# Kernel optimization log

Hardware: AMD Instinct MI355X
Metric: run time of the kernel (lower is better)

The kernel has to match this reference:

```python
import jax, jax.numpy as jnp
import numpy as np
from jax import lax

PATCH = 16
DILATIONS = (1, 2, 4, 8)
R2_THRESH = 0.5


def setup_inputs() -> dict:
    key = jax.random.key(0)
    k1, k2, k3 = jax.random.split(key, 3)
    seasonal = jax.random.normal(k1, (32, 2048, 8), dtype=jnp.float32)
    # 4 Conv1d(1,1,k=16) kernels + biases (PyTorch default init scale ~1/sqrt(k))
    conv_w = jax.random.normal(k2, (4, PATCH), dtype=jnp.float32) / np.sqrt(PATCH).astype(np.float32)
    conv_b = jax.random.normal(k3, (4,), dtype=jnp.float32) * 0.01
    return {"seasonal": seasonal, "conv_w": conv_w, "conv_b": conv_b}


def _r2(y):
    n = y.shape[-1]
    x = jnp.arange(n, dtype=y.dtype)
    xm = x - x.mean()                                  # [2p]
    ym = y - y.mean(axis=-1, keepdims=True)            # [..., 2p]
    sxy = jnp.einsum('...k,k->...', ym, xm)
    sxx = jnp.sum(xm * xm)
    syy = jnp.sum(ym * ym, axis=-1)
    return (sxy * sxy) / (sxx * syy)


def _forward(seasonal, conv_w, conv_b):
    B, S, C = seasonal.shape
    p = PATCH
    # channels are processed independently with the SAME convs -> fuse B and C
    x = seasonal.transpose(0, 2, 1).reshape(B * C, 1, S)  # [BC,1,S]
    win = jnp.arange(S - p + 1)[:, None] + jnp.arange(p)[None, :]  # [n_patches,p]
    cand_list = []
    for i, d in enumerate(DILATIONS):
        pad = (p - 1) * d
        out = lax.conv_general_dilated(
            x, conv_w[i].reshape(1, 1, p), window_strides=(1,),
            padding=[(pad, pad)], rhs_dilation=(d,)) + conv_b[i]
        out = out[:, 0, :S]                      # crop to seq_len, [BC,S]
        cand_list.append(out[:, win])            # sliding windows [BC,n_patches,p]
    cand = jnp.concatenate(cand_list, axis=1)    # [BC,N,p]
    N = cand.shape[1]

    # r^2 score for every adjacent pair (vectorized; greedy scan only gates it)
    pair = jnp.concatenate([cand[:, :-1], cand[:, 1:]], axis=-1)  # [BC,N-1,2p]
    can_merge = jnp.pad(_r2(pair) >= R2_THRESH, ((0, 0), (0, 1)),
                        constant_values=False)   # [BC,N]; last idx never merges

    # greedy sequential merge: if pair (i,i+1) merges, i+1 is consumed
    def step(consumed, cm_i):
        merge = jnp.logical_and(~consumed, cm_i)
        return merge, (merge, ~consumed)

    def scan_one(cm):
        _, (merge, valid) = lax.scan(step, jnp.zeros((), jnp.bool_), cm)
        return merge, valid

    merge, valid = jax.vmap(scan_one)(can_merge)  # [BC,N] each

    nxt = jnp.concatenate([cand[:, 1:], cand[:, -1:]], axis=1)
    outs = jnp.where(merge[..., None], 0.5 * (cand + nxt), cand)  # [BC,N,p]

    # pack selected patches to the front (stable order), zero-pad the tail
    order = jnp.argsort(~valid, axis=1)  # jax argsort is stable; valid first
    packed = jnp.take_along_axis(outs, order[..., None], axis=1)
    vmask = jnp.take_along_axis(valid, order, axis=1)
    packed = packed * vmask[..., None].astype(packed.dtype)

    return packed.reshape(B, C, N, p).transpose(0, 2, 3, 1)  # [B,N,p,C]


def reference(seasonal, conv_w, conv_b):
    return _forward(seasonal, conv_w, conv_b)
```

## Files before the change

### kernel.cpp

```cpp
#include <hip/hip_runtime.h>

#define SLEN 2048
#define PATCH 16
#define ND 4
#define NW 2033
#define NCAND 8132
#define NROWS 256
#define NCH 8
#define ROWPAD 8192


#define CDX(x) ((x) + ((x) >> 4))
#define XSX(x) ((x) + ((x) >> 3))

__global__ __launch_bounds__(512) void k1(
    const float* __restrict__ seasonal,
    const float* __restrict__ conv_w,
    const float* __restrict__ conv_b,
    float* __restrict__ convf,
    unsigned short* __restrict__ sel)
{
    const int row = blockIdx.x;
    const int b = row >> 3, c = row & 7;
    const int tid = threadIdx.x;

    __shared__ float  xs[XSX(SLEN-1)+1];
    __shared__ double cd[CDX(ND*SLEN-1)+1];
    __shared__ unsigned char c0s[512];
    __shared__ int      wmax[8];
    __shared__ unsigned wsum[8];

    for (int j = tid; j < SLEN; j += 512)
        xs[XSX(j)] = seasonal[(size_t)(b*SLEN + j)*NCH + c];
    __syncthreads();

    for (int d = 0; d < ND; ++d) {
        const int dil = 1 << d;
        double w[PATCH];
        #pragma unroll
        for (int k = 0; k < PATCH; ++k) w[k] = (double)conv_w[d*PATCH + k];
        const double bias = (double)conv_b[d];
        const int r  = tid & (dil - 1);
        const int g  = tid >> d;
        const int bx = g*4*dil + r;

        double xt[19];
        #pragma unroll
        for (int q = 0; q < 19; ++q) {
            int idx = bx + (q - 15)*dil;
            xt[q] = (idx >= 0) ? (double)xs[XSX(idx)] : 0.0;
        }
        double acc[4];
        #pragma unroll
        for (int m = 0; m < 4; ++m) acc[m] = 0.0;
        if (g >= 4) {
            #pragma unroll
            for (int m = 0; m < 4; ++m)
                #pragma unroll
                for (int k = 0; k < PATCH; ++k)
                    acc[m] += w[k] * xt[m + k];
        } else {
            #pragma unroll
            for (int m = 0; m < 4; ++m)
                #pragma unroll
                for (int k = 0; k < PATCH; ++k)
                    if (4*g + m + k - 15 >= 0)
                        acc[m] += w[k] * xt[m + k];
        }
        const int ob = d*SLEN + bx;
        #pragma unroll
        for (int m = 0; m < 4; ++m)
            cd[CDX(ob + m*dil)] = acc[m] + bias;
    }
    __syncthreads();

    {
        float* dst = convf + (size_t)row * ROWPAD;
        #pragma unroll
        for (int j = 0; j < 4; ++j) {
            int i4 = (tid + j*512) * 4;
            float4 v;
            v.x = (float)cd[CDX(i4+0)];
            v.y = (float)cd[CDX(i4+1)];
            v.z = (float)cd[CDX(i4+2)];
            v.w = (float)cd[CDX(i4+3)];
            *(float4*)&dst[i4] = v;
        }
    }

    unsigned char* cmL = (unsigned char*)xs;
    {
        const int d  = tid >> 7;
        const int u  = tid & 127;
        const int db = d * SLEN;
        if (u < 127) {
            const int w0 = u * 16;
            double W1=0.0, W2=0.0, Wk=0.0;
            #pragma unroll
            for (int k = 0; k < 16; ++k) {
                double v = cd[CDX(db + w0 + k)];
                W1 += v; W2 = fma(v,v,W2); Wk = fma((double)k,v,Wk);
            }
            unsigned char* crow = cmL + d*NW;
            #pragma unroll
            for (int j = 0; j < 16; ++j) {
                double v0 = cd[CDX(db+w0+j)], v16 = cd[CDX(db+w0+j+16)];
                double nW1 = W1 + (v16 - v0);
                double nW2 = W2 + (v16*v16 - v0*v0);
                double nWk = Wk - W1 + v0 + 15.0*v16;
                double S1  = W1 + nW1;
                double S2  = W2 + nW2;
                double Sxy = (Wk - 15.5*W1) + (nWk + 0.5*nW1);
                double syy = S2 - S1*S1*(1.0/32.0);
                crow[w0+j] = (unsigned char)((Sxy*Sxy >= 1364.0*syy) && (syy > 0.0));
                W1 = nW1; W2 = nW2; Wk = nWk;
            }
        } else if (d < 3) {
            double aW1=0,aW2=0,aWk=0, bW1=0,bW2=0,bWk=0;
            #pragma unroll
            for (int k = 0; k < 16; ++k) {
                double va = cd[CDX(db + 2032 + k)];
                double vb = cd[CDX(db + SLEN + k)];
                aW1 += va; aW2 = fma(va,va,aW2); aWk = fma((double)k,va,aWk);
                bW1 += vb; bW2 = fma(vb,vb,bW2); bWk = fma((double)k,vb,bWk);
            }
            double S1  = aW1 + bW1;
            double S2  = aW2 + bW2;
            double Sxy = (aWk - 15.5*aW1) + (bWk + 0.5*bW1);
            double syy = S2 - S1*S1*(1.0/32.0);
            cmL[d*NW + 2032] = (unsigned char)((Sxy*Sxy >= 1364.0*syy) && (syy > 0.0));
        }
        if (tid < 61) cmL[NCAND - 1 + tid] = 0;
    }
    __syncthreads();

    const int base = tid * 16;
    unsigned cmbits = 0;
    {
        const unsigned* cw = (const unsigned*)cmL;
        #pragma unroll
        for (int q = 0; q < 4; ++q) {
            unsigned wrd = cw[tid*4 + q];
            #pragma unroll
            for (int bb = 0; bb < 4; ++bb) {
                unsigned bit = ((wrd >> (8*bb)) & 0xffu) ? 1u : 0u;
                cmbits |= bit << (q*4 + bb);
            }
        }
    }
    unsigned inv16 = (~cmbits) & 0xffffu;
    const bool allones = (inv16 == 0u);
    unsigned T = allones ? 16u : (unsigned)__clz(inv16 << 16);
    c0s[tid] = (unsigned char)(T & 1u);
    int pm = allones ? -1 : tid;

    const int lane = tid & 63, wid = tid >> 6;
    int mscan = pm;
    #pragma unroll
    for (int off = 1; off < 64; off <<= 1) {
        int v = __shfl_up(mscan, off);
        if (lane >= off && v > mscan) mscan = v;
    }
    if (lane == 63) wmax[wid] = mscan;
    __syncthreads();
    int pshift = __shfl_up(mscan, 1);
    int mexcl = (lane == 0) ? -1 : pshift;
    #pragma unroll
    for (int wq = 0; wq < 8; ++wq)
        if (wq < wid) { int v = wmax[wq]; if (v > mexcl) mexcl = v; }
    unsigned carry = (mexcl >= 0) ? (unsigned)c0s[mexcl] : 0u;

    int nelem = NCAND - base; if (nelem > 16) nelem = 16; if (nelem < 0) nelem = 0;
    unsigned cons = carry, validb = 0, mergeb = 0;
    int cnt = 0;
    for (int w2 = 0; w2 < nelem; ++w2) {
        unsigned bit = (cmbits >> w2) & 1u;
        unsigned val = cons ^ 1u;
        unsigned mrg = bit & val;
        validb |= val << w2;
        mergeb |= mrg << w2;
        cnt += (int)val;
        cons = mrg;
    }

    int sscan = cnt;
    #pragma unroll
    for (int off = 1; off < 64; off <<= 1) {
        int v = __shfl_up(sscan, off);
        if (lane >= off) sscan += v;
    }
    if (lane == 63) wsum[wid] = (unsigned)sscan;
    __syncthreads();
    unsigned wbase = 0, total = 0;
    #pragma unroll
    for (int wq = 0; wq < 8; ++wq) {
        unsigned v = wsum[wq];
        if (wq < wid) wbase += v;
        total += v;
    }
    unsigned r = wbase + (unsigned)(sscan - cnt);

    unsigned short* selrow = sel + (size_t)row * ROWPAD;
    for (int w2 = 0; w2 < nelem; ++w2) {
        if ((validb >> w2) & 1u)
            selrow[r++] = (unsigned short)(((base + w2) << 1) | (int)((mergeb >> w2) & 1u));
    }
    for (int idx = (int)total + tid; idx < NCAND; idx += 512)
        selrow[idx] = 0xFFFFu;
}

__global__ __launch_bounds__(256) void k_out(
    const float* __restrict__ convf,
    const unsigned short* __restrict__ sel,
    float* __restrict__ out)
{
    __shared__ float gbuf[8*132];
    __shared__ int   amin_s[8], amax_s[8];
    __shared__ float tile[32*132];

    const int t = threadIdx.x;
    const int c = t & 7;
    const int s = t >> 3;
    const unsigned bq = blockIdx.x;
    const unsigned b  = bq / 255u;
    const unsigned m  = bq - b*255u;
    const int n0 = (int)m*32;
    const int ns = (NCAND - n0 < 32) ? (NCAND - n0) : 32;
    const unsigned row = b*NCH + (unsigned)c;

    if (t < 8) { amin_s[t] = 0x7fffffff; amax_s[t] = -1; }
    __syncthreads();

    int e = -1, ai = 0, ai2 = 0;
    if (s < ns) {
        unsigned short e16 = sel[(size_t)row*ROWPAD + (n0 + s)];
        e = (e16 == 0xFFFFu) ? -1 : (int)e16;
        if (e >= 0) {
            const int i  = e >> 1;
            const int d  = (i >= 3*NW) ? 3 : (i >= 2*NW) ? 2 : (i >= NW) ? 1 : 0;
            ai = i + 15*d;
            int ae;
            if (e & 1) {
                const int i2 = i + 1;
                const int d2 = (i2 >= 3*NW) ? 3 : (i2 >= 2*NW) ? 2 : (i2 >= NW) ? 1 : 0;
                ai2 = i2 + 15*d2;
                ae = ai2 + 16;
            } else {
                ai2 = ai;
                ae = ai + 16;
            }
            atomicMin(&amin_s[c], ai);
            atomicMax(&amax_s[c], ae);
        }
    }
    __syncthreads();

    {
        const int r = t >> 5, j = t & 31;
        const int lo = amin_s[r], hi = amax_s[r];
        if (lo <= hi) {
            const float* src = convf + (size_t)(b*NCH + r)*8192;
            for (int o = j; o <= hi - lo; o += 32)
                gbuf[r*132 + o] = src[lo + o];
        }
    }
    __syncthreads();

    float vals[16];
    if (e < 0) {
        #pragma unroll
        for (int k = 0; k < 16; ++k) vals[k] = 0.0f;
    } else {
        const float* f = gbuf + c*132 + (ai  - amin_s[c]);
        const float* g = gbuf + c*132 + (ai2 - amin_s[c]);
        if (e & 1) {
            #pragma unroll
            for (int k = 0; k < 16; ++k) vals[k] = 0.5f*(f[k] + g[k]);
        } else {
            #pragma unroll
            for (int k = 0; k < 16; ++k) vals[k] = f[k];
        }
    }
    if (s < ns) {
        float* tr = tile + s*132 + c;
        #pragma unroll
        for (int k = 0; k < 16; ++k) tr[k*8] = vals[k];
    }
    __syncthreads();

    const size_t obase = ((size_t)b*NCAND + n0)*128;
    const int nw = ns*128;
    #pragma unroll
    for (int m2 = 0; m2 < 4; ++m2) {
        int L = (t + m2*256)*4;
        if (L < nw) {
            int s2 = L >> 7, j = L & 127;
            float4 v = *(const float4*)&tile[s2*132 + j];
            *(float4*)&out[obase + L] = v;
        }
    }
}

extern "C" void kernel_launch(void* const* d_in, const int* in_sizes, int n_in,
                              void* d_out, int out_size, void* d_ws, size_t ws_size,
                              hipStream_t stream) {
    const float* seasonal = (const float*)d_in[0];
    const float* conv_w   = (const float*)d_in[1];
    const float* conv_b   = (const float*)d_in[2];
    float* out = (float*)d_out;

    char* ws = (char*)d_ws;
    unsigned short* sel   = (unsigned short*)(ws);
    float*          convf = (float*)(ws + 16777216);

    hipLaunchKernelGGL(k1,    dim3(NROWS), dim3(512), 0, stream,
                       seasonal, conv_w, conv_b, convf, sel);
    hipLaunchKernelGGL(k_out, dim3(32*255), dim3(256), 0, stream,
                       convf, sel, out);
}
```

Baseline: 161.9 us.

## Drop LDS staging in output kernel; read convf and write output directly

Removes the shared-memory gather buffer, the atomic min/max range computation, the transpose tile, and all three block barriers from the output kernel. Each thread now reads its 16 conv values straight from global memory (through cache) and writes them to the output with a stride-8 pattern. Block-level synchronization and LDS traffic go away, but the global stores become scalar and strided across channels instead of coalesced float4 stores. Whether a wavefront's stores still merge into contiguous lines depends on the memory system.

Result: slower. 169.9 us (+4.9%).

```diff
diff --git a/kernel.cpp b/kernel.cpp
--- a/kernel.cpp
+++ b/kernel.cpp
@@ -214,10 +214,6 @@
     const unsigned short* __restrict__ sel,
     float* __restrict__ out)
 {
-    __shared__ float gbuf[8*132];
-    __shared__ int   amin_s[8], amax_s[8];
-    __shared__ float tile[32*132];
-
     const int t = threadIdx.x;
     const int c = t & 7;
     const int s = t >> 3;
@@ -225,79 +221,37 @@
     const unsigned b  = bq / 255u;
     const unsigned m  = bq - b*255u;
     const int n0 = (int)m*32;
-    const int ns = (NCAND - n0 < 32) ? (NCAND - n0) : 32;
+    int n = n0 + s;
+    const bool live = (n < NCAND);
+    if (!live) n = 0;
     const unsigned row = b*NCH + (unsigned)c;
 
-    if (t < 8) { amin_s[t] = 0x7fffffff; amax_s[t] = -1; }
-    __syncthreads();
-
-    int e = -1, ai = 0, ai2 = 0;
-    if (s < ns) {
-        unsigned short e16 = sel[(size_t)row*ROWPAD + (n0 + s)];
-        e = (e16 == 0xFFFFu) ? -1 : (int)e16;
-        if (e >= 0) {
-            const int i  = e >> 1;
-            const int d  = (i >= 3*NW) ? 3 : (i >= 2*NW) ? 2 : (i >= NW) ? 1 : 0;
-            ai = i + 15*d;
-            int ae;
-            if (e & 1) {
-                const int i2 = i + 1;
-                const int d2 = (i2 >= 3*NW) ? 3 : (i2 >= 2*NW) ? 2 : (i2 >= NW) ? 1 : 0;
-                ai2 = i2 + 15*d2;
-                ae = ai2 + 16;
-            } else {
-                ai2 = ai;
-                ae = ai + 16;
-            }
-            atomicMin(&amin_s[c], ai);
-            atomicMax(&amax_s[c], ae);
-        }
-    }
-    __syncthreads();
-
-    {
-        const int r = t >> 5, j = t & 31;
-        const int lo = amin_s[r], hi = amax_s[r];
-        if (lo <= hi) {
-            const float* src = convf + (size_t)(b*NCH + r)*8192;
-            for (int o = j; o <= hi - lo; o += 32)
-                gbuf[r*132 + o] = src[lo + o];
-        }
-    }
-    __syncthreads();
-
+    const unsigned short e16 = sel[(size_t)row*ROWPAD + n];
+    const int e = (e16 == 0xFFFFu) ? -1 : (int)e16;
+
+    const float* frow = convf + (size_t)row*ROWPAD;
     float vals[16];
     if (e < 0) {
         #pragma unroll
         for (int k = 0; k < 16; ++k) vals[k] = 0.0f;
     } else {
-        const float* f = gbuf + c*132 + (ai  - amin_s[c]);
-        const float* g = gbuf + c*132 + (ai2 - amin_s[c]);
+        const int i  = e >> 1;
+        const int d  = (i >= 3*NW) ? 3 : (i >= 2*NW) ? 2 : (i >= NW) ? 1 : 0;
+        const float* f = frow + (i + 15*d);
+        #pragma unroll
+        for (int k = 0; k < 16; ++k) vals[k] = f[k];
         if (e & 1) {
-            #pragma unroll
-            for (int k = 0; k < 16; ++k) vals[k] = 0.5f*(f[k] + g[k]);
-        } else {
-            #pragma unroll
-            for (int k = 0; k < 16; ++k) vals[k] = f[k];
-        }
-    }
-    if (s < ns) {
-        float* tr = tile + s*132 + c;
-        #pragma unroll
-        for (int k = 0; k < 16; ++k) tr[k*8] = vals[k];
-    }
-    __syncthreads();
-
-    const size_t obase = ((size_t)b*NCAND + n0)*128;
-    const int nw = ns*128;
-    #pragma unroll
-    for (int m2 = 0; m2 < 4; ++m2) {
-        int L = (t + m2*256)*4;
-        if (L < nw) {
-            int s2 = L >> 7, j = L & 127;
-            float4 v = *(const float4*)&tile[s2*132 + j];
-            *(float4*)&out[obase + L] = v;
-        }
+            const int i2 = i + 1;
+            const int d2 = (i2 >= 3*NW) ? 3 : (i2 >= 2*NW) ? 2 : (i2 >= NW) ? 1 : 0;
+            const float* g = frow + (i2 + 15*d2);
+            #pragma unroll
+            for (int k = 0; k < 16; ++k) vals[k] = 0.5f*(vals[k] + g[k]);
+        }
+    }
+    if (live) {
+        float* orow = out + ((size_t)b*NCAND + n)*128 + c;
+        #pragma unroll
+        for (int k = 0; k < 16; ++k) orow[k*8] = vals[k];
     }
 }
 
```
